# Kernel optimization log

Hardware: AMD Instinct MI355X
Metric: run time of the kernel (lower is better)

The kernel has to match this reference:

```python
import jax, jax.numpy as jnp
import numpy as np

B, C, H, W = 8, 16, 512, 512


def setup_inputs() -> dict:
    key = jax.random.key(0)
    kx, kr, ki = jax.random.split(key, 3)
    x = jax.random.normal(kx, (B, C, H, W), dtype=jnp.float32)
    H_real = jax.random.normal(kr, (H, W), dtype=jnp.float32)
    H_imag = jax.random.normal(ki, (H, W), dtype=jnp.float32)
    return {"x": x, "H_real": H_real, "H_imag": H_imag}


def reference(x, H_real, H_imag):
    # FFT over the last two (spatial) dims, pointwise complex filter, inverse FFT.
    x_fft = jnp.fft.fft2(x)                       # [B,C,H,W] complex64
    H_complex = jax.lax.complex(H_real, H_imag)   # [H,W] complex64, broadcasts
    y = jnp.fft.ifft2(x_fft * H_complex)
    return jnp.real(y)
```

## Files before the change

### kernel.cpp

```cpp
#include <hip/hip_runtime.h>

__device__ __forceinline__ float2 cmul(float2 a, float2 b) {
    return make_float2(a.x*b.x - a.y*b.y, a.x*b.y + a.y*b.x);
}
__device__ __forceinline__ float2 cadd(float2 a, float2 b){ return make_float2(a.x+b.x, a.y+b.y); }
__device__ __forceinline__ float2 csub(float2 a, float2 b){ return make_float2(a.x-b.x, a.y-b.y); }

__device__ __forceinline__ void wsync() {
    asm volatile("s_waitcnt lgkmcnt(0)" ::: "memory");
}

template<int SGN> __device__ __forceinline__ float2 mul_i(float2 a) {
    return (SGN > 0) ? make_float2(-a.y, a.x) : make_float2(a.y, -a.x);
}
template<int SGN> __device__ __forceinline__ float2 mul_w81(float2 a) {
    const float r = 0.70710678118654752440f;
    return (SGN > 0) ? make_float2(r*(a.x - a.y), r*(a.x + a.y))
                     : make_float2(r*(a.x + a.y), r*(a.y - a.x));
}
template<int SGN> __device__ __forceinline__ float2 mul_w83(float2 a) {
    const float r = 0.70710678118654752440f;
    return (SGN > 0) ? make_float2(-r*(a.x + a.y), r*(a.x - a.y))
                     : make_float2(r*(a.y - a.x), -r*(a.x + a.y));
}

template<int SGN>
__device__ __forceinline__ void bfly8(float2 v[8]) {
    float2 s0 = cadd(v[0], v[4]), d0 = csub(v[0], v[4]);
    float2 s1 = cadd(v[1], v[5]), d1 = csub(v[1], v[5]);
    float2 s2 = cadd(v[2], v[6]), d2 = csub(v[2], v[6]);
    float2 s3 = cadd(v[3], v[7]), d3 = csub(v[3], v[7]);
    d1 = mul_w81<SGN>(d1);
    d2 = mul_i<SGN>(d2);
    d3 = mul_w83<SGN>(d3);
    float2 p0 = cadd(s0, s2), q0 = csub(s0, s2);
    float2 p1 = cadd(s1, s3), q1 = mul_i<SGN>(csub(s1, s3));
    float2 P0 = cadd(d0, d2), Q0 = csub(d0, d2);
    float2 P1 = cadd(d1, d3), Q1 = mul_i<SGN>(csub(d1, d3));
    v[0] = cadd(p0, p1);
    v[4] = csub(p0, p1);
    v[2] = cadd(q0, q1);
    v[6] = csub(q0, q1);
    v[1] = cadd(P0, P1);
    v[5] = csub(P0, P1);
    v[3] = cadd(Q0, Q1);
    v[7] = csub(Q0, Q1);
}

template<int SGN>
__device__ __forceinline__ void twiddle7(float2 v[8], float frac) {
    const float ang = (SGN > 0 ? 6.2831853071795864769f : -6.2831853071795864769f) * frac;
    float sn, cs; __sincosf(ang, &sn, &cs);
    const float2 w1 = make_float2(cs, sn);
    float2 w = w1;
    v[1] = cmul(v[1], w);
#pragma unroll
    for (int q = 2; q < 8; ++q) { w = cmul(w, w1); v[q] = cmul(v[q], w); }
}


__device__ __forceinline__ void fft512_fwd(float2 v[8], float2* S, int l) {
    const int g = l >> 3, j = l & 7;
    bfly8<-1>(v);
    twiddle7<-1>(v, (float)l * (1.0f/512.0f));
#pragma unroll
    for (int q = 0; q < 8; ++q) S[66*q + l] = v[q];
    wsync();
#pragma unroll
    for (int k = 0; k < 8; ++k) v[k] = S[66*g + j + 8*k];
    bfly8<-1>(v);
    twiddle7<-1>(v, (float)j * (1.0f/64.0f));
#pragma unroll
    for (int q = 0; q < 8; ++q) S[72*g + 9*q + j] = v[q];
    wsync();
#pragma unroll
    for (int k = 0; k < 8; ++k) v[k] = S[9*l + k];
    bfly8<-1>(v);
}

__device__ __forceinline__ void fft512_inv(float2 v[8], float2* S, int l) {
    const int g = l >> 3, j = l & 7;
    bfly8<1>(v);
#pragma unroll
    for (int k = 0; k < 8; ++k) S[9*l + k] = v[k];
    wsync();
#pragma unroll
    for (int q = 0; q < 8; ++q) v[q] = S[72*g + 9*q + j];
    twiddle7<1>(v, (float)j * (1.0f/64.0f));
    bfly8<1>(v);
#pragma unroll
    for (int k = 0; k < 8; ++k) S[66*g + j + 8*k] = v[k];
    wsync();
#pragma unroll
    for (int q = 0; q < 8; ++q) v[q] = S[66*q + l];
    twiddle7<1>(v, (float)l * (1.0f/512.0f));
    bfly8<1>(v);
}

__device__ __forceinline__ int drev(int x) {
    return ((x & 7) << 6) | (x & 56) | (x >> 6);
}

__global__ __launch_bounds__(256) void permH(const float* __restrict__ Hr,
                                             const float* __restrict__ Hi,
                                             float2* __restrict__ Hp) {
    const int pw = blockIdx.x;
    const int kw = drev(pw);
    const int nw = (512 - kw) & 511;
    for (int ph = threadIdx.x; ph < 512; ph += 256) {
        const int kh = drev(ph);
        const int nh = (512 - kh) & 511;
        const float hr = 0.5f * (Hr[(kh << 9) + kw] + Hr[(nh << 9) + nw]);
        const float hi = 0.5f * (Hi[(kh << 9) + kw] - Hi[(nh << 9) + nw]);
        Hp[(pw << 9) + ph] = make_float2(hr, hi);
    }
}

__global__ __launch_bounds__(256) void pass1_rows(const float* __restrict__ x,
                                                  float2* __restrict__ ws) {
    __shared__ float2 smem[4 * 577];
    const int t = threadIdx.x;
    const int l = t & 63, w = t >> 6;
    float2* S = smem + w * 577;
    const size_t row = (size_t)blockIdx.x * 4 + w;
    const size_t img = row >> 9;
    const size_t h   = row & 511;
    const float* src1 = x + ((img * 2) << 18) + (h << 9);
    const float* src2 = src1 + (1 << 18);
    float2 v[8];
#pragma unroll
    for (int k = 0; k < 8; ++k) v[k] = make_float2(src1[l + 64*k], src2[l + 64*k]);
    fft512_fwd(v, S, l);
    float4* dst = (float4*)(ws + row * 512 + 8*l);
#pragma unroll
    for (int q = 0; q < 4; ++q)
        dst[q] = make_float4(v[2*q].x, v[2*q].y, v[2*q+1].x, v[2*q+1].y);
}

__global__ __launch_bounds__(512) void pass2_cols(float2* __restrict__ ws,
                                                  const float2* __restrict__ Hp) {
    __shared__ float2 smem[4616];
    const int t = threadIdx.x;
    const int l = t & 63, w = t >> 6;
    const int img = blockIdx.x >> 6;
    const int w0 = (blockIdx.x & 63) * 8;
    float2* base = ws + ((size_t)img << 18) + w0;

    {
        const int c = t & 3, u = t >> 2;
#pragma unroll
        for (int k = 0; k < 4; ++k) {
            int h = u + 128*k;
            float4 p = *(const float4*)(base + (size_t)h * 512 + 2*c);
            smem[9*h + 2*c]     = make_float2(p.x, p.y);
            smem[9*h + 2*c + 1] = make_float2(p.z, p.w);
        }
    }
    __syncthreads();
    float2 v[8];
#pragma unroll
    for (int k = 0; k < 8; ++k) v[k] = smem[9*(l + 64*k) + w];
    __syncthreads();
    float2* S = smem + w * 577;
    fft512_fwd(v, S, l);
    {
        const float4* hp = (const float4*)(Hp + (((size_t)(w0 + w)) << 9) + 8*l);
#pragma unroll
        for (int q = 0; q < 4; ++q) {
            float4 h2 = hp[q];
            v[2*q]   = cmul(v[2*q],   make_float2(h2.x, h2.y));
            v[2*q+1] = cmul(v[2*q+1], make_float2(h2.z, h2.w));
        }
    }
    fft512_inv(v, S, l);
    __syncthreads();
#pragma unroll
    for (int k = 0; k < 8; ++k) smem[9*(l + 64*k) + w] = v[k];
    __syncthreads();
    {
        const int c = t & 3, u = t >> 2;
#pragma unroll
        for (int k = 0; k < 4; ++k) {
            int h = u + 128*k;
            float2 a = smem[9*h + 2*c], b = smem[9*h + 2*c + 1];
            *(float4*)(base + (size_t)h * 512 + 2*c) = make_float4(a.x, a.y, b.x, b.y);
        }
    }
}

__global__ __launch_bounds__(256) void pass3_rows(const float2* __restrict__ ws,
                                                  float* __restrict__ out) {
    __shared__ float2 smem[4 * 577];
    const int t = threadIdx.x;
    const int l = t & 63, w = t >> 6;
    float2* S = smem + w * 577;
    const size_t row = (size_t)blockIdx.x * 4 + w;
    const size_t img = row >> 9;
    const size_t h   = row & 511;
    const float4* src = (const float4*)(ws + row * 512 + 8*l);
    float2 v[8];
#pragma unroll
    for (int q = 0; q < 4; ++q) {
        float4 p = src[q];
        v[2*q]   = make_float2(p.x, p.y);
        v[2*q+1] = make_float2(p.z, p.w);
    }
    fft512_inv(v, S, l);
    const float sc = 1.0f / (512.0f * 512.0f);
    float* dst1 = out + ((img * 2) << 18) + (h << 9);
    float* dst2 = dst1 + (1 << 18);
#pragma unroll
    for (int k = 0; k < 8; ++k) {
        dst1[l + 64*k] = v[k].x * sc;
        dst2[l + 64*k] = v[k].y * sc;
    }
}

extern "C" void kernel_launch(void* const* d_in, const int* in_sizes, int n_in,
                              void* d_out, int out_size, void* d_ws, size_t ws_size,
                              hipStream_t stream) {
    const float* x  = (const float*)d_in[0];
    const float* Hr = (const float*)d_in[1];
    const float* Hi = (const float*)d_in[2];
    float* out = (float*)d_out;
    float2* ws = (float2*)d_ws;
    float2* Hp = (float2*)d_out;

    permH<<<512, 256, 0, stream>>>(Hr, Hi, Hp);
    pass1_rows<<<8192, 256, 0, stream>>>(x, ws);
    pass2_cols<<<4096, 512, 0, stream>>>(ws, Hp);
    pass3_rows<<<8192, 256, 0, stream>>>(ws, out);
}
```

Before: 351.3 us.

## Split three-pass FFT into four image chunks to keep workspace cache-resident

The three row/column/row passes now run over four chunks of 16 complex images each instead of all 64 at once. The aim is a per-chunk workspace small enough (32 MB) to stay resident in the large last-level cache between passes, cutting HBM traffic. The filter table moves from the output buffer to a slot in the workspace so later chunks cannot overwrite it. In exchange there are more kernel launches and fewer blocks per launch, which adds launch overhead and tail effects.

```diff
diff --git a/kernel.cpp b/kernel.cpp
--- a/kernel.cpp
+++ b/kernel.cpp
@@ -116,33 +116,36 @@
     }
 }
 
+
 __global__ __launch_bounds__(256) void pass1_rows(const float* __restrict__ x,
-                                                  float2* __restrict__ ws) {
+                                                  float2* __restrict__ ws,
+                                                  int img0) {
     __shared__ float2 smem[4 * 577];
     const int t = threadIdx.x;
     const int l = t & 63, w = t >> 6;
     float2* S = smem + w * 577;
-    const size_t row = (size_t)blockIdx.x * 4 + w;
-    const size_t img = row >> 9;
-    const size_t h   = row & 511;
+    const size_t r   = (size_t)blockIdx.x * 4 + w;
+    const size_t img = (size_t)img0 + (r >> 9);
+    const size_t h   = r & 511;
     const float* src1 = x + ((img * 2) << 18) + (h << 9);
     const float* src2 = src1 + (1 << 18);
     float2 v[8];
 #pragma unroll
     for (int k = 0; k < 8; ++k) v[k] = make_float2(src1[l + 64*k], src2[l + 64*k]);
     fft512_fwd(v, S, l);
-    float4* dst = (float4*)(ws + row * 512 + 8*l);
+    float4* dst = (float4*)(ws + (img * 512 + h) * 512 + 8*l);
 #pragma unroll
     for (int q = 0; q < 4; ++q)
         dst[q] = make_float4(v[2*q].x, v[2*q].y, v[2*q+1].x, v[2*q+1].y);
 }
 
 __global__ __launch_bounds__(512) void pass2_cols(float2* __restrict__ ws,
-                                                  const float2* __restrict__ Hp) {
+                                                  const float2* __restrict__ Hp,
+                                                  int img0) {
     __shared__ float2 smem[4616];
     const int t = threadIdx.x;
     const int l = t & 63, w = t >> 6;
-    const int img = blockIdx.x >> 6;
+    const int img = img0 + (blockIdx.x >> 6);
     const int w0 = (blockIdx.x & 63) * 8;
     float2* base = ws + ((size_t)img << 18) + w0;
 
@@ -189,15 +192,16 @@
 }
 
 __global__ __launch_bounds__(256) void pass3_rows(const float2* __restrict__ ws,
-                                                  float* __restrict__ out) {
+                                                  float* __restrict__ out,
+                                                  int img0) {
     __shared__ float2 smem[4 * 577];
     const int t = threadIdx.x;
     const int l = t & 63, w = t >> 6;
     float2* S = smem + w * 577;
-    const size_t row = (size_t)blockIdx.x * 4 + w;
-    const size_t img = row >> 9;
-    const size_t h   = row & 511;
-    const float4* src = (const float4*)(ws + row * 512 + 8*l);
+    const size_t r   = (size_t)blockIdx.x * 4 + w;
+    const size_t img = (size_t)img0 + (r >> 9);
+    const size_t h   = r & 511;
+    const float4* src = (const float4*)(ws + (img * 512 + h) * 512 + 8*l);
     float2 v[8];
 #pragma unroll
     for (int q = 0; q < 4; ++q) {
@@ -224,10 +228,13 @@
     const float* Hi = (const float*)d_in[2];
     float* out = (float*)d_out;
     float2* ws = (float2*)d_ws;
-    float2* Hp = (float2*)d_out;
+    float2* Hp = ws + ((size_t)64 << 18);
 
     permH<<<512, 256, 0, stream>>>(Hr, Hi, Hp);
-    pass1_rows<<<8192, 256, 0, stream>>>(x, ws);
-    pass2_cols<<<4096, 512, 0, stream>>>(ws, Hp);
-    pass3_rows<<<8192, 256, 0, stream>>>(ws, out);
-}
+    for (int b = 0; b < 4; ++b) {
+        const int img0 = b * 16;
+        pass1_rows<<<2048, 256, 0, stream>>>(x, ws, img0);
+        pass2_cols<<<1024, 512, 0, stream>>>(ws, Hp, img0);
+        pass3_rows<<<2048, 256, 0, stream>>>(ws, out, img0);
+    }
+}
```

Measured after the change: 402.1 us. +14.4%, slower.
